# Performance work log

Hardware: AMD Instinct MI355X
Metric: run time of the kernel (lower is better)

The kernel has to match this reference:

```python
import jax, jax.numpy as jnp
import numpy as np
from jax import lax

B, S, F = 64, 63, 64          # batch, window length, num_past_features
T, NF, OUT = 12, 63, 1        # pred_sequence_length, forecast feats, output_size
C, K = 32, 3                  # hidden channels, kernel size
DILS = (1, 2, 4, 8, 16)       # S = (K-1)*sum(DILS)+1 = 63 -> conv stack reduces to length 1


def setup_inputs() -> dict:
    key = jax.random.key(0)
    ks = jax.random.split(key, 8)
    sc = 0.1
    x = jax.random.normal(ks[0], (B, S, F), dtype=jnp.float32)
    x_forecasts = jax.random.normal(ks[1], (B, T, NF), dtype=jnp.float32)
    # per-feature conv stacks stored as grouped-conv weights (feature_group_count=F)
    w0 = jax.random.normal(ks[2], (F * C, 1, K), dtype=jnp.float32) * sc
    b0 = jnp.zeros((F * C,), dtype=jnp.float32)
    wmid = jax.random.normal(ks[3], (3, F * C, C, K), dtype=jnp.float32) * sc
    bmid = jnp.zeros((3, F * C), dtype=jnp.float32)
    wlast = jax.random.normal(ks[4], (F * 1, C, K), dtype=jnp.float32) * sc
    blast = jnp.zeros((F,), dtype=jnp.float32)
    linW = jax.random.normal(ks[5], (OUT, F + NF), dtype=jnp.float32) * sc
    linb = jnp.zeros((OUT,), dtype=jnp.float32)
    return dict(x=x, x_forecasts=x_forecasts, w0=w0, b0=b0, wmid=wmid,
                bmid=bmid, wlast=wlast, blast=blast, linW=linW, linb=linb)


def _dconv(h, w, d):
    # h: [B, F*Cin, L]; grouped dilated conv, one group per past feature
    return lax.conv_general_dilated(h, w, window_strides=(1,), padding='VALID',
                                    rhs_dilation=(d,),
                                    dimension_numbers=('NCH', 'OIH', 'NCH'),
                                    feature_group_count=F)


def _step(xw, xf, w0, b0, wmid, bmid, wlast, blast, linW, linb):
    # xw: [B, S, F] window; xf: [B, NF] forecast features for this step
    h = jnp.transpose(xw, (0, 2, 1))                       # [B, F, S]
    h = jax.nn.relu(_dconv(h, w0, DILS[0]) + b0[None, :, None])
    for k in range(3):
        h = jax.nn.relu(_dconv(h, wmid[k], DILS[k + 1]) + bmid[k][None, :, None])
    h = _dconv(h, wlast, DILS[4]) + blast[None, :, None]   # [B, F, 1], no final relu
    feat = jnp.concatenate([h[:, :, 0], xf], axis=1)       # [B, F+NF]
    return feat @ linW.T + linb                            # [B, OUT]


def reference(x, x_forecasts, w0, b0, wmid, bmid, wlast, blast, linW, linb):
    params = (w0, b0, wmid, bmid, wlast, blast, linW, linb)
    out0 = _step(x, x_forecasts[:, 0], *params)

    def body(carry, xs):
        xw, prev = carry
        xf_i, xf_ip1 = xs
        add = jnp.concatenate([xf_i, prev], axis=1)[:, None, :]   # [B,1,F] since NF+OUT=F
        xw = jnp.concatenate([xw[:, 1:, :], add], axis=1)          # slide window
        out = _step(xw, xf_ip1, *params)
        return (xw, out), out

    xs = (jnp.swapaxes(x_forecasts[:, :-1], 0, 1),   # [T-1, B, NF]
          jnp.swapaxes(x_forecasts[:, 1:], 0, 1))
    _, outs = lax.scan(body, (x, out0), xs)          # [T-1, B, OUT]
    return jnp.swapaxes(jnp.concatenate([out0[None], outs], axis=0), 0, 1)  # [B, T, OUT]
```

## Files before the change

### kernel.cpp

```cpp
#include <hip/hip_runtime.h>


typedef _Float16 f16;
typedef _Float16 h2 __attribute__((ext_vector_type(2)));
typedef _Float16 f16x4 __attribute__((ext_vector_type(4)));
typedef _Float16 f16x8 __attribute__((ext_vector_type(8)));
typedef float f32x16 __attribute__((ext_vector_type(16)));

#define OFF_H4    0
#define OFF_ST    49152
#define ST_L0     0
#define ST_L1     128
#define ST_L2     384
#define ST_L3     896
#define ST_STRIDE 1760
#define OFF_H40   161792
#define OFF_RECH  161856
#define OFF_PRM   166464
#define OFF_XFT   167488

#define RECH_N 9216
#define TAIL_N 59392

#define RPAD 36
#define NROW 100

__device__ __forceinline__ void stage_wrow(
    const float* __restrict__ wmid, int m, int f, int tid, f16* wrow)
{
  const float* src = wmid + m * 196608 + f * 3072 + tid * 12;
  f16* dst = wrow + (tid >> 3) * 100 + (tid & 7) * 12;
#pragma unroll
  for (int u = 0; u < 3; ++u) {
    const float4 v = *reinterpret_cast<const float4*>(src + u * 4);
    dst[u * 4 + 0] = (f16)v.x; dst[u * 4 + 1] = (f16)v.y;
    dst[u * 4 + 2] = (f16)v.z; dst[u * 4 + 3] = (f16)v.w;
  }
}

__device__ __forceinline__ void mfma_tile2(
    const f16* IN, f16* OUT, int d, int base,
    const f16* __restrict__ wrow, int lane, const float* sBias)
{
  const int lg = lane >> 5;
  const int co = lane & 31;
  const int col = base + co;

  f16x8 afr[6];
#pragma unroll
  for (int h = 0; h < 2; ++h) {
    const f16* wp = wrow + co * 100 + (h * 16 + lg * 8) * 3;
    f16x4 w4[6];
#pragma unroll
    for (int u = 0; u < 6; ++u) w4[u] = *(const f16x4*)(wp + u * 4);
#pragma unroll
    for (int t = 0; t < 3; ++t)
#pragma unroll
      for (int j = 0; j < 8; ++j) {
        const int o = 3 * j + t;
        afr[t * 2 + h][j] = w4[o >> 2][o & 3];
      }
  }

  f32x16 acc;
#pragma unroll
  for (int r = 0; r < 16; ++r)
    acc[r] = sBias[(r & 3) + 8 * (r >> 2) + 4 * lg];

#pragma unroll
  for (int t = 0; t < 3; ++t) {
#pragma unroll
    for (int h = 0; h < 2; ++h) {
      const f16* bp = IN + (col + t * d) * RPAD + h * 16 + lg * 8;
      f16x4 lo = *(const f16x4*)bp;
      f16x4 hi = *(const f16x4*)(bp + 4);
      f16x8 b = __builtin_shufflevector(lo, hi, 0, 1, 2, 3, 4, 5, 6, 7);
      acc = __builtin_amdgcn_mfma_f32_32x32x16_f16(afr[t * 2 + h], b, acc, 0, 0, 0);
    }
  }

#pragma unroll
  for (int q = 0; q < 4; ++q) {
    const int co0 = q * 8 + 4 * lg;
    f16x4 w;
#pragma unroll
    for (int e = 0; e < 4; ++e)
      w[e] = (f16)fmaxf(acc[q * 4 + e], 0.f);
    *(f16x4*)(OUT + col * RPAD + co0) = w;
  }
}

__global__ __launch_bounds__(256) void tcn_pre(
    const float* __restrict__ x, const float* __restrict__ xfc,
    const float* __restrict__ w0, const float* __restrict__ b0,
    const float* __restrict__ wmid, const float* __restrict__ bmid,
    const float* __restrict__ wlast, const float* __restrict__ blast,
    const float* __restrict__ linW, const float* __restrict__ linb,
    float* __restrict__ ws)
{
  const int blk = blockIdx.x;
  const int tid = threadIdx.x;

  if (blk >= 4096) {
    const int idx = (blk - 4096) * 256 + tid;
    if (idx < RECH_N) {
      const int e = idx & 7, lane = (idx >> 3) & 63, q = idx >> 9;
      const int i = q * 8 + e;
      const int m = i / 48, r2 = i % 48;
      const int k = r2 >> 4, ci = r2 & 15;
      const int c = lane & 31, cib = (lane >> 5) * 16;
      ((f16*)(ws + OFF_RECH))[idx] =
          (f16)wmid[m * 196608 + (2016 + c) * 96 + (cib + ci) * 3 + k];
    } else if (idx < RECH_N + 1024) {
      const int r = idx - RECH_N;
      const int e = r & 3, lane = (r >> 2) & 63, q = r >> 8;
      const int i = q * 4 + e;
      const int c = lane & 31;
      float v = 0.f;
      if (i < 3)        v = w0[(2016 + c) * 3 + i];
      else if (i == 3)  v = b0[2016 + c];
      else if (i < 7)   v = bmid[(i - 4) * 2048 + 2016 + c];
      else if (i < 10)  v = wlast[63 * 96 + c * 3 + (i - 7)];
      else if (i == 10) v = blast[63];
      else if (i == 11) v = linW[63];
      else if (i == 12) v = linb[0];
      ws[OFF_PRM + r] = v;
    } else if (idx < TAIL_N) {
      const int r = idx - (RECH_N + 1024);
      const int b = r / 768, rem = r % 768;
      const int q = rem >> 8, lane = (rem >> 2) & 63, e = rem & 3;
      const int i = q * 4 + e;
      ws[OFF_XFT + r] = (lane < 63 && i < 12) ? xfc[(b * 12 + i) * 63 + lane] : 0.f;
    }
    return;
  }

  const int b = blk >> 6;
  const int f = blk & 63;
  const bool lastf = (f == 63);
  const int lane = tid & 63;
  const int g = __builtin_amdgcn_readfirstlane(tid >> 6);

  __shared__ float sIn[80];
  __shared__ float sBias[3][32];
  __shared__ f16 actA[NROW * RPAD];
  __shared__ f16 actB[NROW * RPAD];
  __shared__ __align__(8) f16 wrow[32 * 100];

  for (int t = tid; t < 80; t += 256) {
    float v = 0.f;
    if (t < 63)                 v = x[(b * 63 + t) * 64 + f];
    else if (t < 74 && !lastf)  v = xfc[(b * 12 + (t - 63)) * 63 + f];
    sIn[t] = v;
  }
  if (tid < 96) sBias[tid >> 5][tid & 31] = bmid[(tid >> 5) * 2048 + f * 32 + (tid & 31)];
  for (int i = tid; i < (NROW - 72) * RPAD; i += 256) actA[72 * RPAD + i] = (f16)0.f;
  for (int i = tid; i < (NROW - 68) * RPAD; i += 256) actB[68 * RPAD + i] = (f16)0.f;
  stage_wrow(wmid, 0, f, tid, wrow);
  __syncthreads();

  {
    const float* wb  = w0 + (f * 32 + g * 8) * 3;
    const float* bbp = b0 + f * 32 + g * 8;
#pragma unroll
    for (int it = 0; it < 2; ++it) {
      const int p = lane + it * 64;
      if (p < 72) {
        const float i0 = sIn[p], i1 = sIn[p + 1], i2 = sIn[p + 2];
        f16x4 wv[2];
#pragma unroll
        for (int j = 0; j < 8; ++j) {
          float v = fmaf(wb[j * 3 + 0], i0,
                    fmaf(wb[j * 3 + 1], i1,
                    fmaf(wb[j * 3 + 2], i2, bbp[j])));
          wv[j >> 2][j & 3] = (f16)fmaxf(v, 0.f);
        }
        *(f16x4*)(actA + p * RPAD + g * 8)     = wv[0];
        *(f16x4*)(actA + p * RPAD + g * 8 + 4) = wv[1];
      }
    }
  }
  __syncthreads();

  float* st = ws + OFF_ST + b * ST_STRIDE;

  if (lastf) {
    for (int t = tid; t < 128; t += 256)
      st[ST_L0 + t] = (float)actA[(57 + (t >> 5)) * RPAD + (t & 31)];
  }
  if (g < 3) mfma_tile2(actA, actB, 2, g * 32, wrow, lane, sBias[0]);
  __syncthreads();

  stage_wrow(wmid, 1, f, tid, wrow);
  if (lastf) {
    for (int t = tid; t < 256; t += 256)
      st[ST_L1 + t] = (float)actB[(49 + (t >> 5)) * RPAD + (t & 31)];
  }
  __syncthreads();

  if (g < 2) mfma_tile2(actB, actA, 4, g * 32, wrow, lane, sBias[1]);
  __syncthreads();

  stage_wrow(wmid, 2, f, tid, wrow);
  if (lastf) {
    for (int t = tid; t < 512; t += 256)
      st[ST_L2 + t] = (float)actA[(33 + (t >> 5)) * RPAD + (t & 31)];
  }
  __syncthreads();

  if (g < 2) mfma_tile2(actA, actB, 8, g * 32, wrow, lane, sBias[2]);
  __syncthreads();

  if (lastf) {
    for (int t = tid; t < 864; t += 256)
      st[ST_L3 + t] = (float)actB[(1 + (t >> 5)) * RPAD + (t & 31)];
  }
  if (tid < 12) {
    const int p = tid;
    float acc = blast[f];
    const float* wl = wlast + f * 96;
#pragma unroll
    for (int k = 0; k < 3; ++k) {
      const int row = p + 16 * k;
#pragma unroll
      for (int ci0 = 0; ci0 < 32; ci0 += 4) {
        f16x4 av = *(const f16x4*)(actB + row * RPAD + ci0);
#pragma unroll
        for (int e = 0; e < 4; ++e)
          acc = fmaf(wl[(ci0 + e) * 3 + k], (float)av[e], acc);
      }
    }
    if (!lastf) {
      ws[OFF_H4 + b * 768 + (p >> 2) * 256 + f * 4 + (p & 3)] = acc;
    } else {
      ws[OFF_H4 + b * 768 + (p >> 2) * 256 + 63 * 4 + (p & 3)] = 0.f;
      if (p == 0) ws[OFF_H40 + b] = acc;
    }
  }
}


__device__ __forceinline__ float fd2(h2 a, h2 b, float c) {
#if __has_builtin(__builtin_amdgcn_fdot2)
  return __builtin_amdgcn_fdot2(a, b, c, false);
#else
  return fmaf((float)a[0], (float)b[0], fmaf((float)a[1], (float)b[1], c));
#endif
}

__device__ __forceinline__ float dotv(f16x8 w, f16x8 a, float acc) {
  h2 w0 = {w[0], w[1]}, a0 = {a[0], a[1]};
  h2 w1 = {w[2], w[3]}, a1 = {a[2], a[3]};
  h2 w2 = {w[4], w[5]}, a2 = {a[4], a[5]};
  h2 w3 = {w[6], w[7]}, a3 = {a[6], a[7]};
  acc = fd2(w0, a0, acc);
  acc = fd2(w1, a1, acc);
  acc = fd2(w2, a2, acc);
  acc = fd2(w3, a3, acc);
  return acc;
}

__device__ __forceinline__ f16x8 combineh(f16x8 lo, f16x8 hi) {
  f16x8 s = lo + hi;
#pragma unroll
  for (int i = 0; i < 8; ++i) s[i] = (s[i] > (f16)0.f) ? s[i] : (f16)0.f;
  return s;
}

__device__ __forceinline__ void load16f(const float* p, float* r) {
  const float4* q = reinterpret_cast<const float4*>(p);
  const float4 v0 = q[0], v1 = q[1], v2 = q[2], v3 = q[3];
  r[0]=v0.x;  r[1]=v0.y;  r[2]=v0.z;  r[3]=v0.w;
  r[4]=v1.x;  r[5]=v1.y;  r[6]=v1.z;  r[7]=v1.w;
  r[8]=v2.x;  r[9]=v2.y;  r[10]=v2.z; r[11]=v2.w;
  r[12]=v3.x; r[13]=v3.y; r[14]=v3.z; r[15]=v3.w;
}

__global__ __launch_bounds__(64, 1) void tcn_seq(
    const float* __restrict__ x,
    const float* __restrict__ linW,
    const float* __restrict__ ws, float* __restrict__ out)
{
  const int b = blockIdx.x;
  const int tid = threadIdx.x;
  const int c = tid & 31;
  const int h = tid >> 5;
  const int cib = h * 16;

  __shared__ __align__(16) f16 L0h[15 * 32];
  __shared__ __align__(16) f16 L1p[2][19 * 32];
  __shared__ __align__(16) f16 L2p[2][27 * 32];
  __shared__ __align__(16) f16 wseqh[18 * 64 * 8];
  __shared__ __align__(16) float qs[32];
  __shared__ float preArr[12];

  const float* stp = ws + OFF_ST + b * ST_STRIDE;

  for (int t = tid; t < 128; t += 64) L0h[t] = (f16)stp[ST_L0 + t];
  for (int t = tid; t < 256; t += 64) { L1p[0][t] = (f16)stp[ST_L1 + t]; L1p[1][t] = (f16)0.f; }
  for (int t = tid; t < 512; t += 64) { L2p[0][t] = (f16)stp[ST_L2 + t]; L2p[1][t] = (f16)0.f; }

  {
    const f16* rech = (const f16*)(ws + OFF_RECH);
#pragma unroll
    for (int q = 0; q < 18; ++q)
      *(f16x8*)(wseqh + (q * 64 + tid) * 8) = *(const f16x8*)(rech + (q * 64 + tid) * 8);
  }

  float prm[16];
  {
    const float* tab = ws + OFF_PRM;
#pragma unroll
    for (int q = 0; q < 4; ++q) {
      const float4 v = *reinterpret_cast<const float4*>(tab + (q * 64 + tid) * 4);
      prm[q * 4 + 0] = v.x; prm[q * 4 + 1] = v.y;
      prm[q * 4 + 2] = v.z; prm[q * 4 + 3] = v.w;
    }
  }
  const float w00 = prm[0],  w01 = prm[1],  w02 = prm[2],  b00 = prm[3];
  const float bm0 = prm[4],  bm1 = prm[5],  bm2 = prm[6];
  const float wl0c = prm[7], wl1c = prm[8], wl2c = prm[9];
  const float bl = prm[10],  lw63 = prm[11], lb0 = prm[12];

  const float xv61 = x[(b * 63 + 61) * 64 + 63];
  const float xv62 = x[(b * 63 + 62) * 64 + 63];
  const float h40v = ws[OFF_H40 + b];

  float accv[12];
  {
    float lw = 0.f, lwx = 0.f;
    if (tid < 63) { lw = linW[tid]; lwx = linW[64 + tid]; }
    float h4v[12], xv[12];
#pragma unroll
    for (int q = 0; q < 3; ++q) {
      const float4 hv  = *reinterpret_cast<const float4*>(ws + OFF_H4 + b * 768 + q * 256 + tid * 4);
      const float4 xvv = *reinterpret_cast<const float4*>(ws + OFF_XFT + b * 768 + q * 256 + tid * 4);
      h4v[q*4+0] = hv.x; h4v[q*4+1] = hv.y; h4v[q*4+2] = hv.z; h4v[q*4+3] = hv.w;
      xv[q*4+0] = xvv.x; xv[q*4+1] = xvv.y; xv[q*4+2] = xvv.z; xv[q*4+3] = xvv.w;
    }
#pragma unroll
    for (int i = 0; i < 12; ++i) accv[i] = fmaf(lw, h4v[i], lwx * xv[i]);

    if (tid < 32) {
#pragma unroll
      for (int i = 1; i < 12; ++i) {
        const float qc = fmaf(wl0c, stp[ST_L3 + (i - 1) * 32 + tid],
                              wl1c * stp[ST_L3 + (i + 15) * 32 + tid]);
        accv[i] = fmaf(lw63, qc, accv[i]);
      }
    }
#pragma unroll
    for (int r = 1; r < 64; r <<= 1) {
#pragma unroll
      for (int i = 0; i < 12; ++i) accv[i] += __shfl_xor(accv[i], r);
    }
  }
  if (tid == 0) {
#pragma unroll
    for (int i = 1; i < 12; ++i) preArr[i] = accv[i] + lb0 + lw63 * bl;
  }
  __syncthreads();

  const f16* wbase = wseqh;
  asm volatile("" : "+v"(wbase));

  const float out0 = fmaf(lw63, h40v, accv[0] + lb0);
  if (tid == 0) out[b * 12 + 0] = out0;
  float o1 = out0, o2 = xv62, o3 = xv61;

#pragma unroll 1
  for (int s = 1; s < 12; ++s) {
    const float preS = preArr[s];

    const float nL0 = fmaxf(fmaf(w00, o3, fmaf(w01, o2, fmaf(w02, o1, b00))), 0.f);
    L0h[(3 + s) * 32 + c] = (f16)nL0;

    float v1;
    {
      const f16* wp = wbase + (0 * 6 * 64 + tid) * 8;
      f16x8 W0 = *(const f16x8*)(wp);
      f16x8 W1 = *(const f16x8*)(wp + 64 * 8);
      f16x8 W2 = *(const f16x8*)(wp + 2 * 64 * 8);
      f16x8 W3 = *(const f16x8*)(wp + 3 * 64 * 8);
      f16x8 W4 = *(const f16x8*)(wp + 4 * 64 * 8);
      f16x8 W5 = *(const f16x8*)(wp + 5 * 64 * 8);
      const f16* r0p = L0h + (s - 1) * 32 + cib;
      const f16* r1p = L0h + (s + 1) * 32 + cib;
      const f16* np  = L0h + (3 + s) * 32 + cib;
      f16x8 R0a = *(const f16x8*)r0p, R0b = *(const f16x8*)(r0p + 8);
      f16x8 R1a = *(const f16x8*)r1p, R1b = *(const f16x8*)(r1p + 8);
      f16x8 Na  = *(const f16x8*)np,  Nb  = *(const f16x8*)(np + 8);
      float a0 = dotv(W0, R0a, 0.f), a1 = dotv(W1, R0b, 0.f);
      a0 = dotv(W2, R1a, a0);        a1 = dotv(W3, R1b, a1);
      a0 = dotv(W4, Na, a0);         a1 = dotv(W5, Nb, a1);
      v1 = a0 + a1 + (h == 0 ? bm0 : 0.f);
    }
    L1p[h][(7 + s) * 32 + c] = (f16)v1;

    float v2;
    {
      const f16* wp = wbase + (1 * 6 * 64 + tid) * 8;
      f16x8 W0 = *(const f16x8*)(wp);
      f16x8 W1 = *(const f16x8*)(wp + 64 * 8);
      f16x8 W2 = *(const f16x8*)(wp + 2 * 64 * 8);
      f16x8 W3 = *(const f16x8*)(wp + 3 * 64 * 8);
      f16x8 W4 = *(const f16x8*)(wp + 4 * 64 * 8);
      f16x8 W5 = *(const f16x8*)(wp + 5 * 64 * 8);
      const int i0 = (s - 1) * 32 + cib, i1 = (s + 3) * 32 + cib, in = (7 + s) * 32 + cib;
      f16x8 R0a = combineh(*(const f16x8*)(&L1p[0][i0]),     *(const f16x8*)(&L1p[1][i0]));
      f16x8 R0b = combineh(*(const f16x8*)(&L1p[0][i0 + 8]), *(const f16x8*)(&L1p[1][i0 + 8]));
      f16x8 R1a = combineh(*(const f16x8*)(&L1p[0][i1]),     *(const f16x8*)(&L1p[1][i1]));
      f16x8 R1b = combineh(*(const f16x8*)(&L1p[0][i1 + 8]), *(const f16x8*)(&L1p[1][i1 + 8]));
      f16x8 Na  = combineh(*(const f16x8*)(&L1p[0][in]),     *(const f16x8*)(&L1p[1][in]));
      f16x8 Nb  = combineh(*(const f16x8*)(&L1p[0][in + 8]), *(const f16x8*)(&L1p[1][in + 8]));
      float a0 = dotv(W0, R0a, 0.f), a1 = dotv(W1, R0b, 0.f);
      a0 = dotv(W2, R1a, a0);        a1 = dotv(W3, R1b, a1);
      a0 = dotv(W4, Na, a0);         a1 = dotv(W5, Nb, a1);
      v2 = a0 + a1 + (h == 0 ? bm1 : 0.f);
    }
    L2p[h][(15 + s) * 32 + c] = (f16)v2;

    float v3;
    {
      const f16* wp = wbase + (2 * 6 * 64 + tid) * 8;
      f16x8 W0 = *(const f16x8*)(wp);
      f16x8 W1 = *(const f16x8*)(wp + 64 * 8);
      f16x8 W2 = *(const f16x8*)(wp + 2 * 64 * 8);
      f16x8 W3 = *(const f16x8*)(wp + 3 * 64 * 8);
      f16x8 W4 = *(const f16x8*)(wp + 4 * 64 * 8);
      f16x8 W5 = *(const f16x8*)(wp + 5 * 64 * 8);
      const int i0 = (s - 1) * 32 + cib, i1 = (s + 7) * 32 + cib, in = (15 + s) * 32 + cib;
      f16x8 R0a = combineh(*(const f16x8*)(&L2p[0][i0]),     *(const f16x8*)(&L2p[1][i0]));
      f16x8 R0b = combineh(*(const f16x8*)(&L2p[0][i0 + 8]), *(const f16x8*)(&L2p[1][i0 + 8]));
      f16x8 R1a = combineh(*(const f16x8*)(&L2p[0][i1]),     *(const f16x8*)(&L2p[1][i1]));
      f16x8 R1b = combineh(*(const f16x8*)(&L2p[0][i1 + 8]), *(const f16x8*)(&L2p[1][i1 + 8]));
      f16x8 Na  = combineh(*(const f16x8*)(&L2p[0][in]),     *(const f16x8*)(&L2p[1][in]));
      f16x8 Nb  = combineh(*(const f16x8*)(&L2p[0][in + 8]), *(const f16x8*)(&L2p[1][in + 8]));
      float a0 = dotv(W0, R0a, 0.f), a1 = dotv(W1, R0b, 0.f);
      a0 = dotv(W2, R1a, a0);        a1 = dotv(W3, R1b, a1);
      a0 = dotv(W4, Na, a0);         a1 = dotv(W5, Nb, a1);
      v3 = a0 + a1 + (h == 0 ? bm2 : 0.f);
    }
    v3 += __shfl_xor(v3, 32);
    const float nL3 = fmaxf(v3, 0.f);

    if (h == 0) qs[c] = wl2c * nL3;
    float qa[16], qb[16];
    load16f(qs, qa); load16f(qs + 16, qb);
    float s0 = 0.f, s1 = 0.f, s2 = 0.f, s3 = 0.f;
#pragma unroll
    for (int i = 0; i < 16; i += 4) {
      s0 += qa[i + 0] + qb[i + 0];
      s1 += qa[i + 1] + qb[i + 1];
      s2 += qa[i + 2] + qb[i + 2];
      s3 += qa[i + 3] + qb[i + 3];
    }
    const float S = (s0 + s1) + (s2 + s3);
    const float outs = fmaf(lw63, S, preS);
    if (tid == 0) out[b * 12 + s] = outs;
    o3 = o2; o2 = o1; o1 = outs;
  }
}


extern "C" void kernel_launch(void* const* d_in, const int* in_sizes, int n_in,
                              void* d_out, int out_size, void* d_ws, size_t ws_size,
                              hipStream_t stream) {
  const float* x     = (const float*)d_in[0];
  const float* xfc   = (const float*)d_in[1];
  const float* w0    = (const float*)d_in[2];
  const float* b0    = (const float*)d_in[3];
  const float* wmid  = (const float*)d_in[4];
  const float* bmid  = (const float*)d_in[5];
  const float* wlast = (const float*)d_in[6];
  const float* blast = (const float*)d_in[7];
  const float* linW  = (const float*)d_in[8];
  const float* linb  = (const float*)d_in[9];
  float* out = (float*)d_out;
  float* ws  = (float*)d_ws;

  tcn_pre<<<4096 + 232, 256, 0, stream>>>(
      x, xfc, w0, b0, wmid, bmid, wlast, blast, linW, linb, ws);
  tcn_seq<<<64, 64, 0, stream>>>(x, linW, ws, out);
}
```

Measured before the change: 41.85 us.

## Precompute old-tap partial dots ahead and compute layer0 redundantly per lane

Splits each layer's dilated conv in the sequential loop into the taps that depend only on older states and the single tap that depends on the newest value. The old-tap partial sums for step s+1 are computed off the critical path, after step s finishes its layer-3 value. Layer 0 is now computed redundantly in registers by every lane from repacked w0/b0 fragments, so layer 1 uses those values directly instead of reading them back from LDS. This shortens the serial dependency chain per step, at the cost of extra register pressure and a larger repack workspace.

New measurement: 42.42 us. No clear change (+1.4%).

```diff
diff --git a/kernel.cpp b/kernel.cpp
--- a/kernel.cpp
+++ b/kernel.cpp
@@ -16,11 +16,11 @@
 #define ST_STRIDE 1760
 #define OFF_H40   161792
 #define OFF_RECH  161856
-#define OFF_PRM   166464
-#define OFF_XFT   167488
-
-#define RECH_N 9216
-#define TAIL_N 59392
+#define OFF_PRM   168512
+#define OFF_XFT   169536
+
+#define RECH_N 13312
+#define TAIL_N 63488
 
 #define RPAD 36
 #define NROW 100
@@ -105,12 +105,22 @@
     const int idx = (blk - 4096) * 256 + tid;
     if (idx < RECH_N) {
       const int e = idx & 7, lane = (idx >> 3) & 63, q = idx >> 9;
-      const int i = q * 8 + e;
-      const int m = i / 48, r2 = i % 48;
-      const int k = r2 >> 4, ci = r2 & 15;
       const int c = lane & 31, cib = (lane >> 5) * 16;
-      ((f16*)(ws + OFF_RECH))[idx] =
-          (f16)wmid[m * 196608 + (2016 + c) * 96 + (cib + ci) * 3 + k];
+      f16 v;
+      if (q < 18) {
+        const int i = q * 8 + e;
+        const int m = i / 48, r2 = i % 48;
+        const int k = r2 >> 4, ci = r2 & 15;
+        v = (f16)wmid[m * 196608 + (2016 + c) * 96 + (cib + ci) * 3 + k];
+      } else if (q < 24) {
+        const int t = q - 18;
+        const int k = t >> 1, ci = cib + (t & 1) * 8 + e;
+        v = (f16)w0[(2016 + ci) * 3 + k];
+      } else {
+        const int ci = cib + (q - 24) * 8 + e;
+        v = (f16)b0[2016 + ci];
+      }
+      ((f16*)(ws + OFF_RECH))[idx] = v;
     } else if (idx < RECH_N + 1024) {
       const int r = idx - RECH_N;
       const int e = r & 3, lane = (r >> 2) & 63, q = r >> 8;
@@ -276,6 +286,57 @@
   r[12]=v3.x; r[13]=v3.y; r[14]=v3.z; r[15]=v3.w;
 }
 
+__device__ __forceinline__ void taps01c(
+    int sn, const f16* __restrict__ wbase, const f16* __restrict__ L0h,
+    const f16 (*__restrict__ L1p)[19 * 32], const f16 (*__restrict__ L2p)[27 * 32],
+    int tid, int cib, float& a1o, float& a2o, float& a3o)
+{
+  {
+    const f16* wp = wbase + tid * 8;
+    f16x8 W0 = *(const f16x8*)(wp);
+    f16x8 W1 = *(const f16x8*)(wp + 64 * 8);
+    f16x8 W2 = *(const f16x8*)(wp + 2 * 64 * 8);
+    f16x8 W3 = *(const f16x8*)(wp + 3 * 64 * 8);
+    const f16* r0p = L0h + (sn - 1) * 32 + cib;
+    const f16* r1p = L0h + (sn + 1) * 32 + cib;
+    f16x8 R0a = *(const f16x8*)r0p, R0b = *(const f16x8*)(r0p + 8);
+    f16x8 R1a = *(const f16x8*)r1p, R1b = *(const f16x8*)(r1p + 8);
+    float p0 = dotv(W0, R0a, 0.f), p1 = dotv(W1, R0b, 0.f);
+    p0 = dotv(W2, R1a, p0);        p1 = dotv(W3, R1b, p1);
+    a1o = p0 + p1;
+  }
+  {
+    const f16* wp = wbase + (6 * 64 + tid) * 8;
+    f16x8 W0 = *(const f16x8*)(wp);
+    f16x8 W1 = *(const f16x8*)(wp + 64 * 8);
+    f16x8 W2 = *(const f16x8*)(wp + 2 * 64 * 8);
+    f16x8 W3 = *(const f16x8*)(wp + 3 * 64 * 8);
+    const int i0 = (sn - 1) * 32 + cib, i1 = (sn + 3) * 32 + cib;
+    f16x8 R0a = combineh(*(const f16x8*)(&L1p[0][i0]),     *(const f16x8*)(&L1p[1][i0]));
+    f16x8 R0b = combineh(*(const f16x8*)(&L1p[0][i0 + 8]), *(const f16x8*)(&L1p[1][i0 + 8]));
+    f16x8 R1a = combineh(*(const f16x8*)(&L1p[0][i1]),     *(const f16x8*)(&L1p[1][i1]));
+    f16x8 R1b = combineh(*(const f16x8*)(&L1p[0][i1 + 8]), *(const f16x8*)(&L1p[1][i1 + 8]));
+    float p0 = dotv(W0, R0a, 0.f), p1 = dotv(W1, R0b, 0.f);
+    p0 = dotv(W2, R1a, p0);        p1 = dotv(W3, R1b, p1);
+    a2o = p0 + p1;
+  }
+  {
+    const f16* wp = wbase + (12 * 64 + tid) * 8;
+    f16x8 W0 = *(const f16x8*)(wp);
+    f16x8 W1 = *(const f16x8*)(wp + 64 * 8);
+    f16x8 W2 = *(const f16x8*)(wp + 2 * 64 * 8);
+    f16x8 W3 = *(const f16x8*)(wp + 3 * 64 * 8);
+    const int i0 = (sn - 1) * 32 + cib, i1 = (sn + 7) * 32 + cib;
+    f16x8 R0a = combineh(*(const f16x8*)(&L2p[0][i0]),     *(const f16x8*)(&L2p[1][i0]));
+    f16x8 R0b = combineh(*(const f16x8*)(&L2p[0][i0 + 8]), *(const f16x8*)(&L2p[1][i0 + 8]));
+    f16x8 R1a = combineh(*(const f16x8*)(&L2p[0][i1]),     *(const f16x8*)(&L2p[1][i1]));
+    f16x8 R1b = combineh(*(const f16x8*)(&L2p[0][i1 + 8]), *(const f16x8*)(&L2p[1][i1 + 8]));
+    float p0 = dotv(W0, R0a, 0.f), p1 = dotv(W1, R0b, 0.f);
+    p0 = dotv(W2, R1a, p0);        p1 = dotv(W3, R1b, p1);
+    a3o = p0 + p1;
+  }
+}
+
 __global__ __launch_bounds__(64, 1) void tcn_seq(
     const float* __restrict__ x,
     const float* __restrict__ linW,
@@ -295,17 +356,22 @@
   __shared__ float preArr[12];
 
   const float* stp = ws + OFF_ST + b * ST_STRIDE;
+  const f16* rech = (const f16*)(ws + OFF_RECH);
 
   for (int t = tid; t < 128; t += 64) L0h[t] = (f16)stp[ST_L0 + t];
   for (int t = tid; t < 256; t += 64) { L1p[0][t] = (f16)stp[ST_L1 + t]; L1p[1][t] = (f16)0.f; }
   for (int t = tid; t < 512; t += 64) { L2p[0][t] = (f16)stp[ST_L2 + t]; L2p[1][t] = (f16)0.f; }
 
-  {
-    const f16* rech = (const f16*)(ws + OFF_RECH);
-#pragma unroll
-    for (int q = 0; q < 18; ++q)
-      *(f16x8*)(wseqh + (q * 64 + tid) * 8) = *(const f16x8*)(rech + (q * 64 + tid) * 8);
-  }
+#pragma unroll
+  for (int q = 0; q < 18; ++q)
+    *(f16x8*)(wseqh + (q * 64 + tid) * 8) = *(const f16x8*)(rech + (q * 64 + tid) * 8);
+
+  f16x8 WL0[6], BL0[2];
+#pragma unroll
+  for (int t = 0; t < 6; ++t)
+    WL0[t] = *(const f16x8*)(rech + ((18 + t) * 64 + tid) * 8);
+  BL0[0] = *(const f16x8*)(rech + (24 * 64 + tid) * 8);
+  BL0[1] = *(const f16x8*)(rech + (25 * 64 + tid) * 8);
 
   float prm[16];
   {
@@ -317,10 +383,10 @@
       prm[q * 4 + 2] = v.z; prm[q * 4 + 3] = v.w;
     }
   }
-  const float w00 = prm[0],  w01 = prm[1],  w02 = prm[2],  b00 = prm[3];
   const float bm0 = prm[4],  bm1 = prm[5],  bm2 = prm[6];
-  const float wl0c = prm[7], wl1c = prm[8], wl2c = prm[9];
+  const float wl2c = prm[9];
   const float bl = prm[10],  lw63 = prm[11], lb0 = prm[12];
+  const float wl0c = prm[7], wl1c = prm[8];
 
   const float xv61 = x[(b * 63 + 61) * 64 + 63];
   const float xv62 = x[(b * 63 + 62) * 64 + 63];
@@ -368,81 +434,65 @@
   if (tid == 0) out[b * 12 + 0] = out0;
   float o1 = out0, o2 = xv62, o3 = xv61;
 
+  float a1, a2, a3;
+  taps01c(1, wbase, L0h, L1p, L2p, tid, cib, a1, a2, a3);
+
 #pragma unroll 1
   for (int s = 1; s < 12; ++s) {
     const float preS = preArr[s];
 
-    const float nL0 = fmaxf(fmaf(w00, o3, fmaf(w01, o2, fmaf(w02, o1, b00))), 0.f);
-    L0h[(3 + s) * 32 + c] = (f16)nL0;
+    f16x8 nl0a, nl0b;
+#pragma unroll
+    for (int e = 0; e < 8; ++e) {
+      const float va = fmaf((float)WL0[0][e], o3,
+                       fmaf((float)WL0[2][e], o2,
+                       fmaf((float)WL0[4][e], o1, (float)BL0[0][e])));
+      const float vb = fmaf((float)WL0[1][e], o3,
+                       fmaf((float)WL0[3][e], o2,
+                       fmaf((float)WL0[5][e], o1, (float)BL0[1][e])));
+      nl0a[e] = (f16)fmaxf(va, 0.f);
+      nl0b[e] = (f16)fmaxf(vb, 0.f);
+    }
+    if ((tid & 31) == 0) {
+      *(f16x8*)(L0h + (3 + s) * 32 + cib)     = nl0a;
+      *(f16x8*)(L0h + (3 + s) * 32 + cib + 8) = nl0b;
+    }
 
     float v1;
     {
-      const f16* wp = wbase + (0 * 6 * 64 + tid) * 8;
-      f16x8 W0 = *(const f16x8*)(wp);
-      f16x8 W1 = *(const f16x8*)(wp + 64 * 8);
-      f16x8 W2 = *(const f16x8*)(wp + 2 * 64 * 8);
-      f16x8 W3 = *(const f16x8*)(wp + 3 * 64 * 8);
-      f16x8 W4 = *(const f16x8*)(wp + 4 * 64 * 8);
-      f16x8 W5 = *(const f16x8*)(wp + 5 * 64 * 8);
-      const f16* r0p = L0h + (s - 1) * 32 + cib;
-      const f16* r1p = L0h + (s + 1) * 32 + cib;
-      const f16* np  = L0h + (3 + s) * 32 + cib;
-      f16x8 R0a = *(const f16x8*)r0p, R0b = *(const f16x8*)(r0p + 8);
-      f16x8 R1a = *(const f16x8*)r1p, R1b = *(const f16x8*)(r1p + 8);
-      f16x8 Na  = *(const f16x8*)np,  Nb  = *(const f16x8*)(np + 8);
-      float a0 = dotv(W0, R0a, 0.f), a1 = dotv(W1, R0b, 0.f);
-      a0 = dotv(W2, R1a, a0);        a1 = dotv(W3, R1b, a1);
-      a0 = dotv(W4, Na, a0);         a1 = dotv(W5, Nb, a1);
-      v1 = a0 + a1 + (h == 0 ? bm0 : 0.f);
+      const f16* wp = wbase + (4 * 64 + tid) * 8;
+      f16x8 W4 = *(const f16x8*)(wp);
+      f16x8 W5 = *(const f16x8*)(wp + 64 * 8);
+      v1 = dotv(W4, nl0a, dotv(W5, nl0b, a1)) + (h == 0 ? bm0 : 0.f);
     }
     L1p[h][(7 + s) * 32 + c] = (f16)v1;
 
     float v2;
     {
-      const f16* wp = wbase + (1 * 6 * 64 + tid) * 8;
-      f16x8 W0 = *(const f16x8*)(wp);
-      f16x8 W1 = *(const f16x8*)(wp + 64 * 8);
-      f16x8 W2 = *(const f16x8*)(wp + 2 * 64 * 8);
-      f16x8 W3 = *(const f16x8*)(wp + 3 * 64 * 8);
-      f16x8 W4 = *(const f16x8*)(wp + 4 * 64 * 8);
-      f16x8 W5 = *(const f16x8*)(wp + 5 * 64 * 8);
-      const int i0 = (s - 1) * 32 + cib, i1 = (s + 3) * 32 + cib, in = (7 + s) * 32 + cib;
-      f16x8 R0a = combineh(*(const f16x8*)(&L1p[0][i0]),     *(const f16x8*)(&L1p[1][i0]));
-      f16x8 R0b = combineh(*(const f16x8*)(&L1p[0][i0 + 8]), *(const f16x8*)(&L1p[1][i0 + 8]));
-      f16x8 R1a = combineh(*(const f16x8*)(&L1p[0][i1]),     *(const f16x8*)(&L1p[1][i1]));
-      f16x8 R1b = combineh(*(const f16x8*)(&L1p[0][i1 + 8]), *(const f16x8*)(&L1p[1][i1 + 8]));
-      f16x8 Na  = combineh(*(const f16x8*)(&L1p[0][in]),     *(const f16x8*)(&L1p[1][in]));
-      f16x8 Nb  = combineh(*(const f16x8*)(&L1p[0][in + 8]), *(const f16x8*)(&L1p[1][in + 8]));
-      float a0 = dotv(W0, R0a, 0.f), a1 = dotv(W1, R0b, 0.f);
-      a0 = dotv(W2, R1a, a0);        a1 = dotv(W3, R1b, a1);
-      a0 = dotv(W4, Na, a0);         a1 = dotv(W5, Nb, a1);
-      v2 = a0 + a1 + (h == 0 ? bm1 : 0.f);
+      const f16* wp = wbase + (10 * 64 + tid) * 8;
+      f16x8 W4 = *(const f16x8*)(wp);
+      f16x8 W5 = *(const f16x8*)(wp + 64 * 8);
+      const int in = (7 + s) * 32 + cib;
+      f16x8 Na = combineh(*(const f16x8*)(&L1p[0][in]),     *(const f16x8*)(&L1p[1][in]));
+      f16x8 Nb = combineh(*(const f16x8*)(&L1p[0][in + 8]), *(const f16x8*)(&L1p[1][in + 8]));
+      v2 = dotv(W4, Na, dotv(W5, Nb, a2)) + (h == 0 ? bm1 : 0.f);
     }
     L2p[h][(15 + s) * 32 + c] = (f16)v2;
 
     float v3;
     {
-      const f16* wp = wbase + (2 * 6 * 64 + tid) * 8;
-      f16x8 W0 = *(const f16x8*)(wp);
-      f16x8 W1 = *(const f16x8*)(wp + 64 * 8);
-      f16x8 W2 = *(const f16x8*)(wp + 2 * 64 * 8);
-      f16x8 W3 = *(const f16x8*)(wp + 3 * 64 * 8);
-      f16x8 W4 = *(const f16x8*)(wp + 4 * 64 * 8);
-      f16x8 W5 = *(const f16x8*)(wp + 5 * 64 * 8);
-      const int i0 = (s - 1) * 32 + cib, i1 = (s + 7) * 32 + cib, in = (15 + s) * 32 + cib;
-      f16x8 R0a = combineh(*(const f16x8*)(&L2p[0][i0]),     *(const f16x8*)(&L2p[1][i0]));
-      f16x8 R0b = combineh(*(const f16x8*)(&L2p[0][i0 + 8]), *(const f16x8*)(&L2p[1][i0 + 8]));
-      f16x8 R1a = combineh(*(const f16x8*)(&L2p[0][i1]),     *(const f16x8*)(&L2p[1][i1]));
-      f16x8 R1b = combineh(*(const f16x8*)(&L2p[0][i1 + 8]), *(const f16x8*)(&L2p[1][i1 + 8]));
-      f16x8 Na  = combineh(*(const f16x8*)(&L2p[0][in]),     *(const f16x8*)(&L2p[1][in]));
-      f16x8 Nb  = combineh(*(const f16x8*)(&L2p[0][in + 8]), *(const f16x8*)(&L2p[1][in + 8]));
-      float a0 = dotv(W0, R0a, 0.f), a1 = dotv(W1, R0b, 0.f);
-      a0 = dotv(W2, R1a, a0);        a1 = dotv(W3, R1b, a1);
-      a0 = dotv(W4, Na, a0);         a1 = dotv(W5, Nb, a1);
-      v3 = a0 + a1 + (h == 0 ? bm2 : 0.f);
+      const f16* wp = wbase + (16 * 64 + tid) * 8;
+      f16x8 W4 = *(const f16x8*)(wp);
+      f16x8 W5 = *(const f16x8*)(wp + 64 * 8);
+      const int in = (15 + s) * 32 + cib;
+      f16x8 Na = combineh(*(const f16x8*)(&L2p[0][in]),     *(const f16x8*)(&L2p[1][in]));
+      f16x8 Nb = combineh(*(const f16x8*)(&L2p[0][in + 8]), *(const f16x8*)(&L2p[1][in + 8]));
+      v3 = dotv(W4, Na, dotv(W5, Nb, a3)) + (h == 0 ? bm2 : 0.f);
     }
     v3 += __shfl_xor(v3, 32);
     const float nL3 = fmaxf(v3, 0.f);
+
+    taps01c(s + 1, wbase, L0h, L1p, L2p, tid, cib, a1, a2, a3);
 
     if (h == 0) qs[c] = wl2c * nL3;
     float qa[16], qb[16];
@@ -479,7 +529,7 @@
   float* out = (float*)d_out;
   float* ws  = (float*)d_ws;
 
-  tcn_pre<<<4096 + 232, 256, 0, stream>>>(
+  tcn_pre<<<4096 + 248, 256, 0, stream>>>(
       x, xfc, w0, b0, wmid, bmid, wlast, blast, linW, linb, ws);
   tcn_seq<<<64, 64, 0, stream>>>(x, linW, ws, out);
 }
```
